# Kernel tuning notes

Hardware: AMD Instinct MI355X
Metric: run time of the kernel (lower is better)

Reference implementation:

```python
import jax, jax.numpy as jnp
import numpy as np

B = 32          # graphs in batch
NP = 1000       # nodes per graph (uniform -> static TopK)
N = B * NP      # total nodes
DEG = 10
E = N * DEG     # intra-graph edges
H, D = 4, 128   # heads, per-head dim (GATConv(32,128,heads=4))
F_IN = 32
HD = H * D      # 512
K = int(np.ceil(0.8 * NP))  # TopKPooling ratio=0.8 -> 800 kept per graph
SLOPE = 0.2     # GATConv leaky_relu negative slope


def setup_inputs() -> dict:
    key = jax.random.key(0)
    ks = jax.random.split(key, 16)
    x = jax.random.normal(ks[0], (N, F_IN), jnp.float32)
    off = (jnp.arange(B, dtype=jnp.int64) * NP)[:, None]
    src = (jax.random.randint(ks[1], (B, NP * DEG), 0, NP) + off).reshape(-1)
    dst = (jax.random.randint(ks[2], (B, NP * DEG), 0, NP) + off).reshape(-1)
    edge_index = jnp.stack([src, dst]).astype(jnp.int64)
    batch = jnp.repeat(jnp.arange(B, dtype=jnp.int64), NP)
    edge_attr = jax.random.normal(ks[3], (E, 16), jnp.float32)
    # GATConv params
    W = jax.random.normal(ks[4], (F_IN, HD), jnp.float32) / np.sqrt(F_IN)
    att_src = jax.random.normal(ks[5], (H, D), jnp.float32) * 0.1
    att_dst = jax.random.normal(ks[6], (H, D), jnp.float32) * 0.1
    bias = jnp.zeros((HD,), jnp.float32)
    # TopKPooling weight
    topk_w = jax.random.normal(ks[7], (HD,), jnp.float32)
    # MLP head
    lin1_w = jax.random.normal(ks[8], (2 * HD, 128), jnp.float32) / np.sqrt(2 * HD)
    lin1_b = jnp.zeros((128,), jnp.float32)
    lin2_w = jax.random.normal(ks[9], (128, 64), jnp.float32) / np.sqrt(128)
    lin2_b = jnp.zeros((64,), jnp.float32)
    lin3_w = jax.random.normal(ks[10], (64, 8), jnp.float32) / np.sqrt(64)
    lin3_b = jnp.zeros((8,), jnp.float32)
    return dict(x=x, edge_index=edge_index, batch=batch, edge_attr=edge_attr,
                W=W, att_src=att_src, att_dst=att_dst, bias=bias, topk_w=topk_w,
                lin1_w=lin1_w, lin1_b=lin1_b, lin2_w=lin2_w, lin2_b=lin2_b,
                lin3_w=lin3_w, lin3_b=lin3_b)


def reference(x, edge_index, batch, edge_attr, W, att_src, att_dst, bias, topk_w,
              lin1_w, lin1_b, lin2_w, lin2_b, lin3_w, lin3_b):
    # ---- GATConv(32,128,heads=4), concat, default self-loops ----
    loop = jnp.arange(N, dtype=edge_index.dtype)
    src = jnp.concatenate([edge_index[0], loop])
    dst = jnp.concatenate([edge_index[1], loop])
    h = (x @ W).reshape(N, H, D)                       # [N,H,D]
    a_s = jnp.einsum('nhd,hd->nh', h, att_src)         # [N,H]
    a_d = jnp.einsum('nhd,hd->nh', h, att_dst)
    e = jax.nn.leaky_relu(a_s[src] + a_d[dst], SLOPE)  # [E2,H]
    m = jax.ops.segment_max(e, dst, num_segments=N)    # per-dst softmax (stable)
    ex = jnp.exp(e - m[dst])
    denom = jax.ops.segment_sum(ex, dst, num_segments=N)
    alpha = ex / denom[dst]                            # [E2,H]
    agg = jax.ops.segment_sum(alpha[:, :, None] * h[src], dst, num_segments=N)
    x1 = jax.nn.relu(agg.reshape(N, HD) + bias)        # [N,512]
    # ---- TopKPooling(512, ratio=0.8), tanh nonlinearity ----
    score = jnp.tanh((x1 @ topk_w) / jnp.linalg.norm(topk_w))  # [N]
    vals, idx = jax.lax.top_k(score.reshape(B, NP), K)         # [B,K]
    xg = x1.reshape(B, NP, HD)
    xs = jnp.take_along_axis(xg, idx[:, :, None], axis=1) * vals[:, :, None]
    # ---- global max + mean pool, MLP head (eval: dropout = identity) ----
    x2 = jnp.concatenate([xs.max(axis=1), xs.mean(axis=1)], axis=-1)  # [B,1024]
    h1 = jax.nn.relu(x2 @ lin1_w + lin1_b)
    h2 = jax.nn.relu(h1 @ lin2_w + lin2_b)
    return jax.nn.log_softmax(h2 @ lin3_w + lin3_b, axis=-1)  # [B,8]
```

## Files before the change

kernel.cpp:

```cpp
#include <hip/hip_runtime.h>
#include <hip/hip_fp16.h>
#include <math.h>


#define N_NODES 32000
#define B_GRAPHS 32
#define NPG 1000
#define DEGC 10
#define E_EDGES (N_NODES*DEGC)
#define HD 512
#define F_IN 32
#define KKEEP 800
#define SLOPE 0.2f
#define CAP 32

__global__ void prep_kernel(const float* __restrict__ W, const float* __restrict__ att_src,
                            const float* __restrict__ att_dst, const float* __restrict__ topk_w,
                            float* __restrict__ Ws, float* __restrict__ Wd, float* __restrict__ misc,
                            int* __restrict__ counts)
{
    int tid = threadIdx.x;
    if (blockIdx.x > 0) {
        int i = (blockIdx.x - 1)*256 + tid;
        if (i < N_NODES/4) ((int4*)counts)[i] = make_int4(0,0,0,0);
        return;
    }
    if (tid < 128) {
        int f = tid >> 2, hh = tid & 3;
        float s1 = 0.f, s2 = 0.f;
        for (int d = 0; d < 128; ++d) {
            float w = W[f*HD + hh*128 + d];
            s1 = fmaf(w, att_src[hh*128 + d], s1);
            s2 = fmaf(w, att_dst[hh*128 + d], s2);
        }
        Ws[f*4+hh] = s1;
        Wd[f*4+hh] = s2;
    }
    __shared__ float red[256];
    float tw0 = topk_w[tid], tw1 = topk_w[tid+256];
    red[tid] = tw0*tw0 + tw1*tw1;
    __syncthreads();
    for (int s = 128; s > 0; s >>= 1) { if (tid < s) red[tid] += red[tid+s]; __syncthreads(); }
    if (tid == 0) misc[0] = 1.0f / sqrtf(red[0]);
}

#define NPB 32
__global__ __launch_bounds__(256) void compute_h_kernel(
    const float* __restrict__ x, const float* __restrict__ W,
    const float* __restrict__ Ws, const float* __restrict__ Wd,
    __half* __restrict__ h, float* __restrict__ a_s, float* __restrict__ a_d)
{
    __shared__ float s_x[NPB*F_IN];
    int tid = threadIdx.x;
    int n0 = blockIdx.x * NPB;
    float wc0[F_IN], wc1[F_IN];
    #pragma unroll
    for (int f = 0; f < F_IN; ++f) {
        float2 wp = *(const float2*)(W + f*HD + 2*tid);
        wc0[f] = wp.x;
        wc1[f] = wp.y;
    }
    const float4* xg = (const float4*)(x + (size_t)n0*F_IN);
    float4* sx4 = (float4*)s_x;
    if (tid < NPB*F_IN/4) sx4[tid] = xg[tid];
    __syncthreads();
    for (int n = 0; n < NPB; ++n) {
        const float4* xr = (const float4*)(s_x + n*F_IN);
        float acc0 = 0.f, acc1 = 0.f;
        #pragma unroll
        for (int f4 = 0; f4 < F_IN/4; ++f4) {
            float4 xv = xr[f4];
            acc0 = fmaf(xv.x, wc0[f4*4+0], acc0); acc1 = fmaf(xv.x, wc1[f4*4+0], acc1);
            acc0 = fmaf(xv.y, wc0[f4*4+1], acc0); acc1 = fmaf(xv.y, wc1[f4*4+1], acc1);
            acc0 = fmaf(xv.z, wc0[f4*4+2], acc0); acc1 = fmaf(xv.z, wc1[f4*4+2], acc1);
            acc0 = fmaf(xv.w, wc0[f4*4+3], acc0); acc1 = fmaf(xv.w, wc1[f4*4+3], acc1);
        }
        *(__half2*)(h + (size_t)(n0+n)*HD + 2*tid) = __floats2half2_rn(acc0, acc1);
    }
    {
        int n = tid >> 3, hh = (tid >> 1) & 3, which = tid & 1;
        const float* Wx = which ? Wd : Ws;
        const float* xr = s_x + n*F_IN;
        float s = 0.f;
        #pragma unroll
        for (int f = 0; f < F_IN; ++f) s = fmaf(xr[f], Wx[f*4+hh], s);
        float* dp = which ? a_d : a_s;
        dp[(size_t)(n0+n)*4 + hh] = s;
    }
}

__global__ void build_slots_kernel(const int* __restrict__ dst, int* __restrict__ counts,
                                   int* __restrict__ slots)
{
    int i = blockIdx.x*blockDim.x + threadIdx.x;
    int stride = gridDim.x*blockDim.x;
    for (; i < E_EDGES; i += stride) {
        int d = dst[i];
        int p = atomicAdd(&counts[d], 1);
        if (p < CAP) slots[d*CAP + p] = i;
    }
}

__global__ __launch_bounds__(256) void gat_agg_kernel(
    const __half* __restrict__ h, const float* __restrict__ a_s, const float* __restrict__ a_d,
    const int* __restrict__ counts, const int* __restrict__ slots, const int* __restrict__ esrc,
    const float* __restrict__ bias, const float* __restrict__ topk_w, const float* __restrict__ misc,
    __half* __restrict__ x1, float* __restrict__ scores)
{
    __shared__ int    s_src[4][CAP];
    __shared__ float4 s_al[4][CAP];
    int tid = threadIdx.x;
    int wid = tid >> 6, lane = tid & 63;
    int grp  = (blockIdx.x & 7) * 1000 + (blockIdx.x >> 3);
    int node = grp*4 + wid;
    int deg  = min(counts[node], CAP);

    int key = (lane < deg) ? slots[node*CAP + lane] : (0x7FFF0000 + lane);
    int rank = 0;
    for (int j = 0; j < deg; ++j) rank += (__shfl(key, j, 64) < key);
    if (lane >= deg) rank = lane;
    int sorted_eid = __builtin_amdgcn_ds_permute(rank << 2, key);

    int src = node;
    if (lane < deg) src = esrc[sorted_eid];

    float4 ad    = *(const float4*)(a_d + (size_t)node*4);
    float4 aself = *(const float4*)(a_s + (size_t)node*4);
    float4 asrc  = make_float4(0.f,0.f,0.f,0.f);
    if (lane < deg) asrc = *(const float4*)(a_s + (size_t)src*4);

    float ex[4], exs[4];
    {
        float u;
        u = asrc.x + ad.x;  ex[0]  = u > 0.f ? u : SLOPE*u;
        u = asrc.y + ad.y;  ex[1]  = u > 0.f ? u : SLOPE*u;
        u = asrc.z + ad.z;  ex[2]  = u > 0.f ? u : SLOPE*u;
        u = asrc.w + ad.w;  ex[3]  = u > 0.f ? u : SLOPE*u;
        u = aself.x + ad.x; exs[0] = __expf(u > 0.f ? u : SLOPE*u);
        u = aself.y + ad.y; exs[1] = __expf(u > 0.f ? u : SLOPE*u);
        u = aself.z + ad.z; exs[2] = __expf(u > 0.f ? u : SLOPE*u);
        u = aself.w + ad.w; exs[3] = __expf(u > 0.f ? u : SLOPE*u);
    }
    float al[4], alself[4];
    #pragma unroll
    for (int hh = 0; hh < 4; ++hh) {
        float e = (lane < deg) ? __expf(ex[hh]) : 0.f;
        float den = e;
        #pragma unroll
        for (int msk = 1; msk < 64; msk <<= 1) den += __shfl_xor(den, msk, 64);
        den += exs[hh];
        float inv = __builtin_amdgcn_rcpf(den);
        al[hh]     = e * inv;
        alself[hh] = exs[hh] * inv;
    }
    if (lane < deg) {
        s_src[wid][lane] = src;
        s_al[wid][lane]  = make_float4(al[0], al[1], al[2], al[3]);
    }
    __syncthreads();

    int c0 = lane*4, c1 = 256 + lane*4;
    bool hi = lane >= 32;
    float f0=0.f,f1=0.f,f2=0.f,f3=0.f,f4=0.f,f5=0.f,f6=0.f,f7=0.f;
    #define MIX_LO(ACC,A,Q) asm("v_fma_mix_f32 %0, %1, %2, %0 op_sel_hi:[0,1,0]" : "+v"(ACC) : "v"(A), "v"(Q))
    #define MIX_HI(ACC,A,Q) asm("v_fma_mix_f32 %0, %1, %2, %0 op_sel:[0,1,0] op_sel_hi:[0,1,0]" : "+v"(ACC) : "v"(A), "v"(Q))
    #define EDGE_STEP(E_IDX)                                                          \
        {   int se = s_src[wid][E_IDX];                                               \
            float4 a4 = s_al[wid][E_IDX];                                             \
            float a0 = hi ? a4.y : a4.x;                                              \
            float a1 = hi ? a4.w : a4.z;                                              \
            uint2 q0 = *(const uint2*)(h + (size_t)se*HD + c0);                       \
            uint2 q1 = *(const uint2*)(h + (size_t)se*HD + c1);                       \
            MIX_LO(f0, a0, q0.x); MIX_HI(f1, a0, q0.x);                               \
            MIX_LO(f2, a0, q0.y); MIX_HI(f3, a0, q0.y);                               \
            MIX_LO(f4, a1, q1.x); MIX_HI(f5, a1, q1.x);                               \
            MIX_LO(f6, a1, q1.y); MIX_HI(f7, a1, q1.y); }
    int e = 0;
    for (; e + 2 <= deg; e += 2) { EDGE_STEP(e); EDGE_STEP(e+1); }
    if (e < deg) EDGE_STEP(e);
    {
        float a0 = hi ? alself[1] : alself[0];
        float a1 = hi ? alself[3] : alself[2];
        uint2 q0 = *(const uint2*)(h + (size_t)node*HD + c0);
        uint2 q1 = *(const uint2*)(h + (size_t)node*HD + c1);
        MIX_LO(f0, a0, q0.x); MIX_HI(f1, a0, q0.x);
        MIX_LO(f2, a0, q0.y); MIX_HI(f3, a0, q0.y);
        MIX_LO(f4, a1, q1.x); MIX_HI(f5, a1, q1.x);
        MIX_LO(f6, a1, q1.y); MIX_HI(f7, a1, q1.y);
    }
    #undef EDGE_STEP
    #undef MIX_LO
    #undef MIX_HI

    float4 b0 = *(const float4*)(bias + c0);
    float4 b1 = *(const float4*)(bias + c1);
    float4 v0, v1;
    v0.x = fmaxf(f0 + b0.x, 0.f); v0.y = fmaxf(f1 + b0.y, 0.f);
    v0.z = fmaxf(f2 + b0.z, 0.f); v0.w = fmaxf(f3 + b0.w, 0.f);
    v1.x = fmaxf(f4 + b1.x, 0.f); v1.y = fmaxf(f5 + b1.y, 0.f);
    v1.z = fmaxf(f6 + b1.z, 0.f); v1.w = fmaxf(f7 + b1.w, 0.f);
    {
        __half2 p0 = __floats2half2_rn(v0.x, v0.y);
        __half2 p1 = __floats2half2_rn(v0.z, v0.w);
        __half2 p2 = __floats2half2_rn(v1.x, v1.y);
        __half2 p3 = __floats2half2_rn(v1.z, v1.w);
        __half2* xp0 = (__half2*)(x1 + (size_t)node*HD + c0);
        __half2* xp1 = (__half2*)(x1 + (size_t)node*HD + c1);
        xp0[0] = p0; xp0[1] = p1;
        xp1[0] = p2; xp1[1] = p3;
    }

    float4 tw0 = *(const float4*)(topk_w + c0);
    float4 tw1 = *(const float4*)(topk_w + c1);
    float p = v0.x*tw0.x + v0.y*tw0.y + v0.z*tw0.z + v0.w*tw0.w
            + v1.x*tw1.x + v1.y*tw1.y + v1.z*tw1.z + v1.w*tw1.w;
    #pragma unroll
    for (int msk = 1; msk < 64; msk <<= 1) p += __shfl_xor(p, msk, 64);
    if (lane == 0) {
        float dotv = p * misc[0];
        float eu   = __expf(2.f * fabsf(dotv));
        float th   = 1.f - 2.f/(eu + 1.f);
        scores[node] = copysignf(th, dotv);
    }
}

__global__ __launch_bounds__(256) void topk_kernel(const float* __restrict__ scores,
                                                   int* __restrict__ kept_ids,
                                                   float* __restrict__ kept_vals)
{
    int g = blockIdx.x, part = blockIdx.y;
    __shared__ float s[NPG];
    int tid = threadIdx.x;
    for (int i = tid; i < NPG; i += 256) s[i] = scores[g*NPG + i];
    __syncthreads();
    int i = part*250 + tid;
    if (tid < 250) {
        float si = s[i];
        int rank = 0;
        for (int j = 0; j < NPG; ++j) {
            float sj = s[j];
            rank += (sj > si) || (sj == si && j < i);
        }
        if (rank < KKEEP) {
            kept_ids[g*KKEEP + rank]  = g*NPG + i;
            kept_vals[g*KKEEP + rank] = si;
        }
    }
}

#define RCHUNK 50
#define NCHUNK 16
__global__ __launch_bounds__(128) void pool_partial_kernel(
    const __half* __restrict__ x1, const int* __restrict__ kept_ids,
    const float* __restrict__ kept_vals, float* __restrict__ pmax, float* __restrict__ psum)
{
    int bid = blockIdx.x;
    int k = bid & 7, q = bid >> 3;
    int g = k*4 + (q & 3), c = q >> 2;
    int tid = threadIdx.x;
    __shared__ int   ids[RCHUNK];
    __shared__ float vals[RCHUNK];
    if (tid < RCHUNK) {
        ids[tid]  = kept_ids[g*KKEEP + c*RCHUNK + tid];
        vals[tid] = kept_vals[g*KKEEP + c*RCHUNK + tid];
    }
    __syncthreads();
    float4 mxA = make_float4(-INFINITY,-INFINITY,-INFINITY,-INFINITY), mxB = mxA;
    float4 smA = make_float4(0.f,0.f,0.f,0.f), smB = smA;
    for (int r = 0; r < RCHUNK; r += 2) {
        const __half2* pA = (const __half2*)(x1 + (size_t)ids[r]*HD + tid*4);
        const __half2* pB = (const __half2*)(x1 + (size_t)ids[r+1]*HD + tid*4);
        __half2 qA0 = pA[0], qA1 = pA[1], qB0 = pB[0], qB1 = pB[1];
        float2 a0 = __half22float2(qA0), a1 = __half22float2(qA1);
        float2 b0 = __half22float2(qB0), b1 = __half22float2(qB1);
        float lA = vals[r], lB = vals[r+1];
        float4 vA = make_float4(a0.x*lA, a0.y*lA, a1.x*lA, a1.y*lA);
        float4 vB = make_float4(b0.x*lB, b0.y*lB, b1.x*lB, b1.y*lB);
        mxA.x = fmaxf(mxA.x, vA.x); mxA.y = fmaxf(mxA.y, vA.y);
        mxA.z = fmaxf(mxA.z, vA.z); mxA.w = fmaxf(mxA.w, vA.w);
        mxB.x = fmaxf(mxB.x, vB.x); mxB.y = fmaxf(mxB.y, vB.y);
        mxB.z = fmaxf(mxB.z, vB.z); mxB.w = fmaxf(mxB.w, vB.w);
        smA.x += vA.x; smA.y += vA.y; smA.z += vA.z; smA.w += vA.w;
        smB.x += vB.x; smB.y += vB.y; smB.z += vB.z; smB.w += vB.w;
    }
    float4 mx, sm;
    mx.x = fmaxf(mxA.x, mxB.x); mx.y = fmaxf(mxA.y, mxB.y);
    mx.z = fmaxf(mxA.z, mxB.z); mx.w = fmaxf(mxA.w, mxB.w);
    sm.x = smA.x + smB.x; sm.y = smA.y + smB.y;
    sm.z = smA.z + smB.z; sm.w = smA.w + smB.w;
    *(float4*)(pmax + (size_t)(g*NCHUNK + c)*HD + tid*4) = mx;
    *(float4*)(psum + (size_t)(g*NCHUNK + c)*HD + tid*4) = sm;
}

__global__ __launch_bounds__(256) void mlp_kernel(
    const float* __restrict__ pmax, const float* __restrict__ psum,
    const float* __restrict__ w1, const float* __restrict__ b1,
    const float* __restrict__ w2, const float* __restrict__ b2,
    const float* __restrict__ w3, const float* __restrict__ b3,
    float* __restrict__ out)
{
    int g = blockIdx.x;
    int tid = threadIdx.x;
    __shared__ float sx[1024];
    __shared__ float part1[8][128];
    __shared__ float sh1[128];
    __shared__ float part2[4][64];
    __shared__ float sh2[64];
    __shared__ float part3[8][8];
    __shared__ float slog[8];

    {
        int half = tid >> 7;
        int c4 = tid & 127;
        const float* basep = half ? psum : pmax;
        float4 r = *(const float4*)(basep + (size_t)(g*NCHUNK)*HD + c4*4);
        #pragma unroll
        for (int c = 1; c < NCHUNK; ++c) {
            float4 v = *(const float4*)(basep + (size_t)(g*NCHUNK + c)*HD + c4*4);
            if (half) { r.x += v.x; r.y += v.y; r.z += v.z; r.w += v.w; }
            else {
                r.x = fmaxf(r.x, v.x); r.y = fmaxf(r.y, v.y);
                r.z = fmaxf(r.z, v.z); r.w = fmaxf(r.w, v.w);
            }
        }
        if (half) { const float inv = 1.0f/KKEEP; r.x *= inv; r.y *= inv; r.z *= inv; r.w *= inv; }
        *(float4*)(sx + half*512 + c4*4) = r;
    }
    __syncthreads();

    {
        int ks = tid >> 5, tc = tid & 31;
        const float* w1p = w1 + (size_t)(ks*128)*128 + tc*4;
        const float* sxp = sx + ks*128;
        float4 acc = make_float4(0.f,0.f,0.f,0.f);
        #pragma unroll 8
        for (int k = 0; k < 128; ++k) {
            float xk = sxp[k];
            float4 w = *(const float4*)(w1p + (size_t)k*128);
            acc.x = fmaf(xk, w.x, acc.x); acc.y = fmaf(xk, w.y, acc.y);
            acc.z = fmaf(xk, w.z, acc.z); acc.w = fmaf(xk, w.w, acc.w);
        }
        *(float4*)(&part1[ks][tc*4]) = acc;
    }
    __syncthreads();
    if (tid < 128) {
        float s = b1[tid];
        #pragma unroll
        for (int p = 0; p < 8; ++p) s += part1[p][tid];
        sh1[tid] = fmaxf(s, 0.0f);
    }
    __syncthreads();

    {
        int ks2 = tid >> 6, to = tid & 63;
        float a = 0.f;
        #pragma unroll 8
        for (int k = 0; k < 32; ++k) {
            int kk = ks2*32 + k;
            a = fmaf(sh1[kk], w2[kk*64 + to], a);
        }
        part2[ks2][to] = a;
    }
    __syncthreads();
    if (tid < 64) {
        float s = b2[tid];
        #pragma unroll
        for (int p = 0; p < 4; ++p) s += part2[p][tid];
        sh2[tid] = fmaxf(s, 0.0f);
    }
    __syncthreads();

    if (tid < 64) {
        int ks3 = tid >> 3, o = tid & 7;
        float a = 0.f;
        #pragma unroll
        for (int k = 0; k < 8; ++k) {
            int kk = ks3*8 + k;
            a = fmaf(sh2[kk], w3[kk*8 + o], a);
        }
        part3[ks3][o] = a;
    }
    __syncthreads();
    if (tid < 8) {
        float s = b3[tid];
        #pragma unroll
        for (int p = 0; p < 8; ++p) s += part3[p][tid];
        slog[tid] = s;
    }
    __syncthreads();
    if (tid == 0) {
        float m = slog[0];
        for (int i = 1; i < 8; ++i) m = fmaxf(m, slog[i]);
        float ssum = 0.0f;
        for (int i = 0; i < 8; ++i) ssum += expf(slog[i] - m);
        float lse = m + logf(ssum);
        for (int i = 0; i < 8; ++i) out[g*8 + i] = slog[i] - lse;
    }
}

extern "C" void kernel_launch(void* const* d_in, const int* in_sizes, int n_in,
                              void* d_out, int out_size, void* d_ws, size_t ws_size,
                              hipStream_t stream) {
    const float* x        = (const float*)d_in[0];
    const int*   ei       = (const int*)d_in[1];
    const float* W        = (const float*)d_in[4];
    const float* att_src  = (const float*)d_in[5];
    const float* att_dst  = (const float*)d_in[6];
    const float* bias     = (const float*)d_in[7];
    const float* topk_w   = (const float*)d_in[8];
    const float* w1       = (const float*)d_in[9];
    const float* b1       = (const float*)d_in[10];
    const float* w2       = (const float*)d_in[11];
    const float* b2       = (const float*)d_in[12];
    const float* w3       = (const float*)d_in[13];
    const float* b3       = (const float*)d_in[14];
    float* out = (float*)d_out;

    const int* src = ei;
    const int* dst = ei + E_EDGES;

    char* wsb = (char*)d_ws;
    size_t off = 0;
    auto alloc = [&](size_t bytes) -> void* {
        void* p = (void*)(wsb + off);
        off += (bytes + 255) & ~(size_t)255;
        return p;
    };
    __half* h       = (__half*)alloc((size_t)N_NODES*HD*2);
    __half* x1      = (__half*)alloc((size_t)N_NODES*HD*2);
    float* a_s      = (float*)alloc((size_t)N_NODES*4*4);
    float* a_d      = (float*)alloc((size_t)N_NODES*4*4);
    float* Ws       = (float*)alloc(F_IN*4*4);
    float* Wd       = (float*)alloc(F_IN*4*4);
    float* misc     = (float*)alloc(256);
    int*   counts   = (int*)alloc((size_t)N_NODES*4);
    int*   slots    = (int*)alloc((size_t)N_NODES*CAP*4);
    float* scores   = (float*)alloc((size_t)N_NODES*4);
    int*   kept_ids = (int*)alloc((size_t)B_GRAPHS*KKEEP*4);
    float* kept_vals= (float*)alloc((size_t)B_GRAPHS*KKEEP*4);
    float* pmax     = (float*)alloc((size_t)B_GRAPHS*NCHUNK*HD*4);
    float* psum     = (float*)alloc((size_t)B_GRAPHS*NCHUNK*HD*4);

    prep_kernel<<<33, 256, 0, stream>>>(W, att_src, att_dst, topk_w, Ws, Wd, misc, counts);
    compute_h_kernel<<<N_NODES/NPB, 256, 0, stream>>>(x, W, Ws, Wd, h, a_s, a_d);
    build_slots_kernel<<<640, 256, 0, stream>>>(dst, counts, slots);
    gat_agg_kernel<<<N_NODES/4, 256, 0, stream>>>(h, a_s, a_d, counts, slots, src,
                                                  bias, topk_w, misc, x1, scores);
    topk_kernel<<<dim3(B_GRAPHS, 4), 256, 0, stream>>>(scores, kept_ids, kept_vals);
    pool_partial_kernel<<<B_GRAPHS*NCHUNK, 128, 0, stream>>>(x1, kept_ids, kept_vals, pmax, psum);
    mlp_kernel<<<B_GRAPHS, 256, 0, stream>>>(pmax, psum, w1, b1, w2, b2, w3, b3, out);
}
```

Measured before the change: 140.7 us.

## Fuse feature transform with edge slot building; widen gather loads per lane

```diff
diff --git a/kernel.cpp b/kernel.cpp
--- a/kernel.cpp
+++ b/kernel.cpp
@@ -45,59 +45,62 @@
 }
 
 #define NPB 32
-__global__ __launch_bounds__(256) void compute_h_kernel(
+#define CH_BLOCKS 1000
+#define BS_BLOCKS 128
+__global__ __launch_bounds__(256) void stage1_kernel(
     const float* __restrict__ x, const float* __restrict__ W,
     const float* __restrict__ Ws, const float* __restrict__ Wd,
-    __half* __restrict__ h, float* __restrict__ a_s, float* __restrict__ a_d)
-{
-    __shared__ float s_x[NPB*F_IN];
-    int tid = threadIdx.x;
-    int n0 = blockIdx.x * NPB;
-    float wc0[F_IN], wc1[F_IN];
-    #pragma unroll
-    for (int f = 0; f < F_IN; ++f) {
-        float2 wp = *(const float2*)(W + f*HD + 2*tid);
-        wc0[f] = wp.x;
-        wc1[f] = wp.y;
-    }
-    const float4* xg = (const float4*)(x + (size_t)n0*F_IN);
-    float4* sx4 = (float4*)s_x;
-    if (tid < NPB*F_IN/4) sx4[tid] = xg[tid];
-    __syncthreads();
-    for (int n = 0; n < NPB; ++n) {
-        const float4* xr = (const float4*)(s_x + n*F_IN);
-        float acc0 = 0.f, acc1 = 0.f;
-        #pragma unroll
-        for (int f4 = 0; f4 < F_IN/4; ++f4) {
-            float4 xv = xr[f4];
-            acc0 = fmaf(xv.x, wc0[f4*4+0], acc0); acc1 = fmaf(xv.x, wc1[f4*4+0], acc1);
-            acc0 = fmaf(xv.y, wc0[f4*4+1], acc0); acc1 = fmaf(xv.y, wc1[f4*4+1], acc1);
-            acc0 = fmaf(xv.z, wc0[f4*4+2], acc0); acc1 = fmaf(xv.z, wc1[f4*4+2], acc1);
-            acc0 = fmaf(xv.w, wc0[f4*4+3], acc0); acc1 = fmaf(xv.w, wc1[f4*4+3], acc1);
-        }
-        *(__half2*)(h + (size_t)(n0+n)*HD + 2*tid) = __floats2half2_rn(acc0, acc1);
-    }
-    {
-        int n = tid >> 3, hh = (tid >> 1) & 3, which = tid & 1;
-        const float* Wx = which ? Wd : Ws;
-        const float* xr = s_x + n*F_IN;
-        float s = 0.f;
-        #pragma unroll
-        for (int f = 0; f < F_IN; ++f) s = fmaf(xr[f], Wx[f*4+hh], s);
-        float* dp = which ? a_d : a_s;
-        dp[(size_t)(n0+n)*4 + hh] = s;
-    }
-}
-
-__global__ void build_slots_kernel(const int* __restrict__ dst, int* __restrict__ counts,
-                                   int* __restrict__ slots)
-{
-    int i = blockIdx.x*blockDim.x + threadIdx.x;
-    int stride = gridDim.x*blockDim.x;
-    for (; i < E_EDGES; i += stride) {
-        int d = dst[i];
-        int p = atomicAdd(&counts[d], 1);
-        if (p < CAP) slots[d*CAP + p] = i;
+    const int* __restrict__ dst,
+    __half* __restrict__ h, float* __restrict__ a_s, float* __restrict__ a_d,
+    int* __restrict__ counts, int* __restrict__ slots)
+{
+    int b = blockIdx.x;
+    int tid = threadIdx.x;
+    if (b < CH_BLOCKS) {
+        __shared__ float s_x[NPB*F_IN];
+        int n0 = (b & 7)*4000 + (b >> 3)*NPB;
+        float wc0[F_IN], wc1[F_IN];
+        #pragma unroll
+        for (int f = 0; f < F_IN; ++f) {
+            float2 wp = *(const float2*)(W + f*HD + 2*tid);
+            wc0[f] = wp.x;
+            wc1[f] = wp.y;
+        }
+        const float4* xg = (const float4*)(x + (size_t)n0*F_IN);
+        float4* sx4 = (float4*)s_x;
+        if (tid < NPB*F_IN/4) sx4[tid] = xg[tid];
+        __syncthreads();
+        for (int n = 0; n < NPB; ++n) {
+            const float4* xr = (const float4*)(s_x + n*F_IN);
+            float acc0 = 0.f, acc1 = 0.f;
+            #pragma unroll
+            for (int f4 = 0; f4 < F_IN/4; ++f4) {
+                float4 xv = xr[f4];
+                acc0 = fmaf(xv.x, wc0[f4*4+0], acc0); acc1 = fmaf(xv.x, wc1[f4*4+0], acc1);
+                acc0 = fmaf(xv.y, wc0[f4*4+1], acc0); acc1 = fmaf(xv.y, wc1[f4*4+1], acc1);
+                acc0 = fmaf(xv.z, wc0[f4*4+2], acc0); acc1 = fmaf(xv.z, wc1[f4*4+2], acc1);
+                acc0 = fmaf(xv.w, wc0[f4*4+3], acc0); acc1 = fmaf(xv.w, wc1[f4*4+3], acc1);
+            }
+            *(__half2*)(h + (size_t)(n0+n)*HD + 2*tid) = __floats2half2_rn(acc0, acc1);
+        }
+        {
+            int n = tid >> 3, hh = (tid >> 1) & 3, which = tid & 1;
+            const float* Wx = which ? Wd : Ws;
+            const float* xr = s_x + n*F_IN;
+            float s = 0.f;
+            #pragma unroll
+            for (int f = 0; f < F_IN; ++f) s = fmaf(xr[f], Wx[f*4+hh], s);
+            float* dp = which ? a_d : a_s;
+            dp[(size_t)(n0+n)*4 + hh] = s;
+        }
+    } else {
+        int i = (b - CH_BLOCKS)*256 + tid;
+        int stride = BS_BLOCKS*256;
+        for (; i < E_EDGES; i += stride) {
+            int d = dst[i];
+            int p = atomicAdd(&counts[d], 1);
+            if (p < CAP) slots[d*CAP + p] = i;
+        }
     }
 }
 
@@ -108,7 +111,7 @@
     __half* __restrict__ x1, float* __restrict__ scores)
 {
     __shared__ int    s_src[4][CAP];
-    __shared__ float4 s_al[4][CAP];
+    __shared__ float4 s_al4[4][CAP];
     int tid = threadIdx.x;
     int wid = tid >> 6, lane = tid & 63;
     int grp  = (blockIdx.x & 7) * 1000 + (blockIdx.x >> 3);
@@ -155,65 +158,63 @@
     }
     if (lane < deg) {
         s_src[wid][lane] = src;
-        s_al[wid][lane]  = make_float4(al[0], al[1], al[2], al[3]);
-    }
-    __syncthreads();
-
-    int c0 = lane*4, c1 = 256 + lane*4;
-    bool hi = lane >= 32;
+        s_al4[wid][lane] = make_float4(al[0], al[1], al[2], al[3]);
+    }
+    __syncthreads();
+
+    int head = lane >> 4;
+    const __half* hb = h + lane*8;
+    const float* alw = (const float*)&s_al4[wid][0];
     float f0=0.f,f1=0.f,f2=0.f,f3=0.f,f4=0.f,f5=0.f,f6=0.f,f7=0.f;
     #define MIX_LO(ACC,A,Q) asm("v_fma_mix_f32 %0, %1, %2, %0 op_sel_hi:[0,1,0]" : "+v"(ACC) : "v"(A), "v"(Q))
     #define MIX_HI(ACC,A,Q) asm("v_fma_mix_f32 %0, %1, %2, %0 op_sel:[0,1,0] op_sel_hi:[0,1,0]" : "+v"(ACC) : "v"(A), "v"(Q))
     #define EDGE_STEP(E_IDX)                                                          \
         {   int se = s_src[wid][E_IDX];                                               \
-            float4 a4 = s_al[wid][E_IDX];                                             \
-            float a0 = hi ? a4.y : a4.x;                                              \
-            float a1 = hi ? a4.w : a4.z;                                              \
-            uint2 q0 = *(const uint2*)(h + (size_t)se*HD + c0);                       \
-            uint2 q1 = *(const uint2*)(h + (size_t)se*HD + c1);                       \
-            MIX_LO(f0, a0, q0.x); MIX_HI(f1, a0, q0.x);                               \
-            MIX_LO(f2, a0, q0.y); MIX_HI(f3, a0, q0.y);                               \
-            MIX_LO(f4, a1, q1.x); MIX_HI(f5, a1, q1.x);                               \
-            MIX_LO(f6, a1, q1.y); MIX_HI(f7, a1, q1.y); }
+            float av = alw[(E_IDX)*4 + head];                                         \
+            uint4 q = *(const uint4*)(hb + (size_t)se*HD);                            \
+            MIX_LO(f0, av, q.x); MIX_HI(f1, av, q.x);                                 \
+            MIX_LO(f2, av, q.y); MIX_HI(f3, av, q.y);                                 \
+            MIX_LO(f4, av, q.z); MIX_HI(f5, av, q.z);                                 \
+            MIX_LO(f6, av, q.w); MIX_HI(f7, av, q.w); }
     int e = 0;
     for (; e + 2 <= deg; e += 2) { EDGE_STEP(e); EDGE_STEP(e+1); }
     if (e < deg) EDGE_STEP(e);
-    {
-        float a0 = hi ? alself[1] : alself[0];
-        float a1 = hi ? alself[3] : alself[2];
-        uint2 q0 = *(const uint2*)(h + (size_t)node*HD + c0);
-        uint2 q1 = *(const uint2*)(h + (size_t)node*HD + c1);
-        MIX_LO(f0, a0, q0.x); MIX_HI(f1, a0, q0.x);
-        MIX_LO(f2, a0, q0.y); MIX_HI(f3, a0, q0.y);
-        MIX_LO(f4, a1, q1.x); MIX_HI(f5, a1, q1.x);
-        MIX_LO(f6, a1, q1.y); MIX_HI(f7, a1, q1.y);
-    }
     #undef EDGE_STEP
+    {
+        float a01 = (head & 1) ? alself[1] : alself[0];
+        float a23 = (head & 1) ? alself[3] : alself[2];
+        float av  = (head & 2) ? a23 : a01;
+        uint4 q = *(const uint4*)(hb + (size_t)node*HD);
+        MIX_LO(f0, av, q.x); MIX_HI(f1, av, q.x);
+        MIX_LO(f2, av, q.y); MIX_HI(f3, av, q.y);
+        MIX_LO(f4, av, q.z); MIX_HI(f5, av, q.z);
+        MIX_LO(f6, av, q.w); MIX_HI(f7, av, q.w);
+    }
     #undef MIX_LO
     #undef MIX_HI
 
+    int c0 = lane*8;
     float4 b0 = *(const float4*)(bias + c0);
-    float4 b1 = *(const float4*)(bias + c1);
-    float4 v0, v1;
-    v0.x = fmaxf(f0 + b0.x, 0.f); v0.y = fmaxf(f1 + b0.y, 0.f);
-    v0.z = fmaxf(f2 + b0.z, 0.f); v0.w = fmaxf(f3 + b0.w, 0.f);
-    v1.x = fmaxf(f4 + b1.x, 0.f); v1.y = fmaxf(f5 + b1.y, 0.f);
-    v1.z = fmaxf(f6 + b1.z, 0.f); v1.w = fmaxf(f7 + b1.w, 0.f);
-    {
-        __half2 p0 = __floats2half2_rn(v0.x, v0.y);
-        __half2 p1 = __floats2half2_rn(v0.z, v0.w);
-        __half2 p2 = __floats2half2_rn(v1.x, v1.y);
-        __half2 p3 = __floats2half2_rn(v1.z, v1.w);
-        __half2* xp0 = (__half2*)(x1 + (size_t)node*HD + c0);
-        __half2* xp1 = (__half2*)(x1 + (size_t)node*HD + c1);
-        xp0[0] = p0; xp0[1] = p1;
-        xp1[0] = p2; xp1[1] = p3;
+    float4 b1 = *(const float4*)(bias + c0 + 4);
+    float v0 = fmaxf(f0 + b0.x, 0.f), v1 = fmaxf(f1 + b0.y, 0.f);
+    float v2 = fmaxf(f2 + b0.z, 0.f), v3 = fmaxf(f3 + b0.w, 0.f);
+    float v4 = fmaxf(f4 + b1.x, 0.f), v5 = fmaxf(f5 + b1.y, 0.f);
+    float v6 = fmaxf(f6 + b1.z, 0.f), v7 = fmaxf(f7 + b1.w, 0.f);
+    {
+        __half2 p0 = __floats2half2_rn(v0, v1);
+        __half2 p1 = __floats2half2_rn(v2, v3);
+        __half2 p2 = __floats2half2_rn(v4, v5);
+        __half2 p3 = __floats2half2_rn(v6, v7);
+        uint4 pk;
+        pk.x = *(unsigned*)&p0; pk.y = *(unsigned*)&p1;
+        pk.z = *(unsigned*)&p2; pk.w = *(unsigned*)&p3;
+        *(uint4*)(x1 + (size_t)node*HD + c0) = pk;
     }
 
     float4 tw0 = *(const float4*)(topk_w + c0);
-    float4 tw1 = *(const float4*)(topk_w + c1);
-    float p = v0.x*tw0.x + v0.y*tw0.y + v0.z*tw0.z + v0.w*tw0.w
-            + v1.x*tw1.x + v1.y*tw1.y + v1.z*tw1.z + v1.w*tw1.w;
+    float4 tw1 = *(const float4*)(topk_w + c0 + 4);
+    float p = v0*tw0.x + v1*tw0.y + v2*tw0.z + v3*tw0.w
+            + v4*tw1.x + v5*tw1.y + v6*tw1.z + v7*tw1.w;
     #pragma unroll
     for (int msk = 1; msk < 64; msk <<= 1) p += __shfl_xor(p, msk, 64);
     if (lane == 0) {
@@ -442,8 +443,8 @@
     float* psum     = (float*)alloc((size_t)B_GRAPHS*NCHUNK*HD*4);
 
     prep_kernel<<<33, 256, 0, stream>>>(W, att_src, att_dst, topk_w, Ws, Wd, misc, counts);
-    compute_h_kernel<<<N_NODES/NPB, 256, 0, stream>>>(x, W, Ws, Wd, h, a_s, a_d);
-    build_slots_kernel<<<640, 256, 0, stream>>>(dst, counts, slots);
+    stage1_kernel<<<CH_BLOCKS + BS_BLOCKS, 256, 0, stream>>>(
+        x, W, Ws, Wd, dst, h, a_s, a_d, counts, slots);
     gat_agg_kernel<<<N_NODES/4, 256, 0, stream>>>(h, a_s, a_d, counts, slots, src,
                                                   bias, topk_w, misc, x1, scores);
     topk_kernel<<<dim3(B_GRAPHS, 4), 256, 0, stream>>>(scores, kept_ids, kept_vals);
```

Measured after the change: 119.3 us, median of 2. -15.2%, faster.
